# Performance work log

Measured on AMD Instinct MI355X. Metric: run time of the kernel, lower is better.

Reference implementation:

```python
import jax, jax.numpy as jnp
import numpy as np
from jax import lax

B, SEQ, PRED, CIN = 32, 336, 336, 7
ALL = SEQ + PRED
DM, DFF, NFFT, WIN, HOP = 64, 64, 64, 64, 8
NF = ALL // HOP + 1  # 85 STFT frames (center=True)
EL, CL, MARK = 2, 3, 4


def _conv2d(x, w, b, dil, pad):
    y = lax.conv_general_dilated(x, w, (1, 1), [(pad, pad), (pad, pad)],
                                 rhs_dilation=(dil, dil),
                                 dimension_numbers=('NCHW', 'OIHW', 'NCHW'))
    return y + b[None, :, None, None]


def _cconv(xr, xi, wr, wi, br, bi, dil, pad):
    # complex conv: (conv_r + i*conv_i)(xr + i*xi)
    rr = _conv2d(xr, wr, br, dil, pad)
    ii = _conv2d(xi, wi, bi, dil, pad)
    ri = _conv2d(xi, wr, br, dil, pad)
    ir = _conv2d(xr, wi, bi, dil, pad)
    return rr - ii, ri + ir


def _block(x, p):
    # x: [B, ALL, DM]; STFT per channel series (vectorized over B*DM, no python batch loop)
    xp = jnp.pad(x.transpose(0, 2, 1), ((0, 0), (0, 0), (NFFT // 2, NFFT // 2)), mode='reflect')
    idx = jnp.arange(NF)[:, None] * HOP + jnp.arange(NFFT)[None, :]
    win = 0.5 - 0.5 * jnp.cos(2.0 * jnp.pi * jnp.arange(WIN, dtype=jnp.float32) / WIN)  # periodic hann
    frames = xp[:, :, idx] * win  # [B, DM, NF, NFFT]
    S = jnp.fft.fft(frames, axis=-1) / jnp.sqrt(jnp.float32(NFFT))  # normalized=True (ortho)
    Sr = S.real.transpose(0, 1, 3, 2).astype(jnp.float32)  # [B, DM, NFFT, NF]
    Si = S.imag.transpose(0, 1, 3, 2).astype(jnp.float32)
    # complex 'qk' attention: compl_mul1d('ijxk,ijyk->ijxy', S, S)
    qk_r = jnp.einsum('bnxk,bnyk->bnxy', Sr, Sr) - jnp.einsum('bnxk,bnyk->bnxy', Si, Si)
    qk_i = jnp.einsum('bnxk,bnyk->bnxy', Sr, Si) + jnp.einsum('bnxk,bnyk->bnxy', Si, Sr)
    g_r = jax.nn.sigmoid(qk_r)
    g_i = jax.nn.sigmoid(qk_i)
    ar = jnp.einsum('bnxy,bnyz->bnxz', g_r, Sr) - jnp.einsum('bnxy,bnyz->bnxz', g_i, Si)
    ai = jnp.einsum('bnxy,bnyz->bnxz', g_r, Si) + jnp.einsum('bnxy,bnyz->bnxz', g_i, Sr)
    outs_r, outs_i = [], []
    yr, yi = _cconv(ar, ai, p['c0_wr'], p['c0_wi'], p['c0_br'], p['c0_bi'], 1, 0)
    outs_r.append(jax.nn.relu(yr)); outs_i.append(jax.nn.relu(yi))
    for k in range(1, CL):
        hr, hi = _cconv(ar, ai, p['cA_wr'][k - 1], p['cA_wi'][k - 1], p['cA_br'][k - 1], p['cA_bi'][k - 1], k, k)
        yr, yi = _cconv(hr, hi, p['cB_wr'][k - 1], p['cB_wi'][k - 1], p['cB_br'][k - 1], p['cB_bi'][k - 1], k, k)
        outs_r.append(jax.nn.relu(yr)); outs_i.append(jax.nn.relu(yi))
    mr = jnp.mean(jnp.stack(outs_r, -1), -1)
    mi = jnp.mean(jnp.stack(outs_i, -1), -1)
    y = mr * p['l0_w'][0, 0] + mi * p['l0_w'][0, 1] + p['l0_b'][0]  # Linear(2 -> 1) over (real, imag)
    y = y.mean(axis=2)  # mean over freq axis -> [B, DM, NF]
    y = jnp.einsum('bnf,af->bna', y, p['l2_w']) + p['l2_b']  # l2: NF -> ALL
    return y.transpose(0, 2, 1)  # [B, ALL, DM]


def _ln(x, g, b):
    m = x.mean(-1, keepdims=True)
    v = ((x - m) ** 2).mean(-1, keepdims=True)
    return (x - m) / jnp.sqrt(v + 1e-5) * g + b


def _forward(x_enc, x_mark_enc, tok_w, temp_w, pl_w, pl_b, ln_g, ln_b,
             c0_wr, c0_wi, c0_br, c0_bi, cA_wr, cA_wi, cA_br, cA_bi,
             cB_wr, cB_wi, cB_br, cB_bi, l0_w, l0_b, l2_w, l2_b,
             cv_w, cv_b, l1_w, l1_b, proj_w, proj_b):
    means = x_enc.mean(1, keepdims=True)
    xe = x_enc - means
    stdev = jnp.sqrt(xe.var(axis=1, keepdims=True) + 1e-5)
    xe = xe / stdev
    # DataEmbedding: circular token conv + sinusoidal PE + timeF linear (dropout=0)
    xv = jnp.pad(xe.transpose(0, 2, 1), ((0, 0), (0, 0), (1, 1)), mode='wrap')
    val = lax.conv_general_dilated(xv, tok_w, (1,), [(0, 0)],
                                   dimension_numbers=('NCH', 'OIH', 'NCH')).transpose(0, 2, 1)
    pos = jnp.arange(SEQ, dtype=jnp.float32)[:, None]
    div = jnp.exp(jnp.arange(0, DM, 2, dtype=jnp.float32) * (-np.log(10000.0) / DM))
    pe = jnp.zeros((SEQ, DM), jnp.float32).at[:, 0::2].set(jnp.sin(pos * div)).at[:, 1::2].set(jnp.cos(pos * div))
    enc = val + x_mark_enc @ temp_w.T + pe
    enc = jnp.einsum('btd,at->bad', enc, pl_w) + pl_b[None, :, None]  # predict_linear over time axis
    for l in range(EL):
        p = dict(c0_wr=c0_wr[l], c0_wi=c0_wi[l], c0_br=c0_br[l], c0_bi=c0_bi[l],
                 cA_wr=cA_wr[l], cA_wi=cA_wi[l], cA_br=cA_br[l], cA_bi=cA_bi[l],
                 cB_wr=cB_wr[l], cB_wi=cB_wi[l], cB_br=cB_br[l], cB_bi=cB_bi[l],
                 l0_w=l0_w[l], l0_b=l0_b[l], l2_w=l2_w[l], l2_b=l2_b[l])
        enc = _ln(_block(enc, p), ln_g, ln_b)
    # conv1d(in=ALL channels, kernel 3, stride 2, pad 1) over the d_model axis, then l1
    h = lax.conv_general_dilated(enc, cv_w, (2,), [(1, 1)],
                                 dimension_numbers=('NCH', 'OIH', 'NCH')) + cv_b[None, :, None]
    seq_series = (h @ l1_w.T)[..., 0] + l1_b[0]  # [B, ALL]
    dec = enc @ proj_w.T + proj_b
    dec = dec * stdev + means
    return dec[:, -PRED:, :], seq_series


def setup_inputs():
    key = jax.random.key(0)
    ks = jax.random.split(key, 24)
    def r(i, shape, s=0.02):
        return jax.random.normal(ks[i], shape, dtype=jnp.float32) * s
    return {
        'x_enc': jax.random.normal(ks[0], (B, SEQ, CIN), dtype=jnp.float32),
        'x_mark_enc': jax.random.normal(ks[1], (B, SEQ, MARK), dtype=jnp.float32),
        'x_dec': jax.random.normal(ks[2], (B, 48 + PRED, CIN), dtype=jnp.float32),
        'x_mark_dec': jax.random.normal(ks[3], (B, 48 + PRED, MARK), dtype=jnp.float32),
        'tok_w': r(4, (DM, CIN, 3), 0.1),
        'temp_w': r(5, (DM, MARK), 0.1),
        'pl_w': r(6, (ALL, SEQ), 0.05),
        'pl_b': jnp.zeros((ALL,), jnp.float32),
        'ln_g': jnp.ones((DM,), jnp.float32),
        'ln_b': jnp.zeros((DM,), jnp.float32),
        'c0_wr': r(7, (EL, DM, DM, 1, 1), 0.05),
        'c0_wi': r(8, (EL, DM, DM, 1, 1), 0.05),
        'c0_br': jnp.zeros((EL, DM), jnp.float32),
        'c0_bi': jnp.zeros((EL, DM), jnp.float32),
        'cA_wr': r(9, (EL, CL - 1, DFF, DM, 3, 3), 0.02),
        'cA_wi': r(10, (EL, CL - 1, DFF, DM, 3, 3), 0.02),
        'cA_br': jnp.zeros((EL, CL - 1, DFF), jnp.float32),
        'cA_bi': jnp.zeros((EL, CL - 1, DFF), jnp.float32),
        'cB_wr': r(11, (EL, CL - 1, DM, DFF, 3, 3), 0.02),
        'cB_wi': r(12, (EL, CL - 1, DM, DFF, 3, 3), 0.02),
        'cB_br': jnp.zeros((EL, CL - 1, DM), jnp.float32),
        'cB_bi': jnp.zeros((EL, CL - 1, DM), jnp.float32),
        'l0_w': r(13, (EL, 1, 2), 0.5),
        'l0_b': jnp.zeros((EL, 1), jnp.float32),
        'l2_w': r(14, (EL, ALL, NF), 0.05),
        'l2_b': jnp.zeros((EL, ALL), jnp.float32),
        'cv_w': r(15, (ALL, ALL, 3), 0.02),
        'cv_b': jnp.zeros((ALL,), jnp.float32),
        'l1_w': r(16, (1, DM // 2), 0.1),
        'l1_b': jnp.zeros((1,), jnp.float32),
        'proj_w': r(17, (CIN, DM), 0.1),
        'proj_b': jnp.zeros((CIN,), jnp.float32),
    }


def reference(x_enc, x_mark_enc, x_dec, x_mark_dec, tok_w, temp_w, pl_w, pl_b, ln_g, ln_b,
              c0_wr, c0_wi, c0_br, c0_bi, cA_wr, cA_wi, cA_br, cA_bi,
              cB_wr, cB_wi, cB_br, cB_bi, l0_w, l0_b, l2_w, l2_b,
              cv_w, cv_b, l1_w, l1_b, proj_w, proj_b):
    del x_dec, x_mark_dec  # unused in the forecast path
    return _forward(x_enc, x_mark_enc, tok_w, temp_w, pl_w, pl_b, ln_g, ln_b,
                    c0_wr, c0_wi, c0_br, c0_bi, cA_wr, cA_wi, cA_br, cA_bi,
                    cB_wr, cB_wi, cB_br, cB_bi, l0_w, l0_b, l2_w, l2_b,
                    cv_w, cv_b, l1_w, l1_b, proj_w, proj_b)
```

## Files before the change

kernel.cpp:

```cpp
#include <hip/hip_runtime.h>

typedef __attribute__((ext_vector_type(8))) short short8v;
typedef __attribute__((ext_vector_type(4))) float f32x4;
typedef __attribute__((ext_vector_type(16))) float f32x16;

static constexpr int Bt = 32;
static constexpr int SEQ = 336, PRED = 336, CIN = 7, ALLT = 672;
static constexpr int DM = 64, NFFT = 64, HOP = 8, NF = 85;
static constexpr int FPAD = 100;
static constexpr int MARK = 4;
static constexpr float INV3 = 1.0f / 3.0f;

__device__ inline short f2bf(float v) {
    unsigned u = __float_as_uint(v);
    u += 0x7fffu + ((u >> 16) & 1u);
    return (short)(u >> 16);
}
__device__ inline float bf2f(short h) {
    return __uint_as_float(((unsigned)(unsigned short)h) << 16);
}
__device__ inline int pack2(float r, float i) {
    return ((int)(unsigned short)f2bf(r)) | (((int)(unsigned short)f2bf(i)) << 16);
}
__device__ inline void async16(const int* g, short* l) {
    __builtin_amdgcn_global_load_lds(
        (const __attribute__((address_space(1))) unsigned int*)g,
        (__attribute__((address_space(3))) unsigned int*)l, 16, 0, 0);
}

__global__ __launch_bounds__(64) void k_stats(const float* __restrict__ x,
                                              float* __restrict__ mean,
                                              float* __restrict__ stdv) {
    int bc = blockIdx.x;
    int b = bc / CIN, c = bc % CIN;
    int lane = threadIdx.x;
    float s = 0.f, s2 = 0.f;
    for (int t = lane; t < SEQ; t += 64) {
        float v = x[(b * SEQ + t) * CIN + c];
        s += v; s2 += v * v;
    }
    for (int m = 32; m >= 1; m >>= 1) { s += __shfl_xor(s, m); s2 += __shfl_xor(s2, m); }
    if (lane == 0) {
        float mu = s / SEQ;
        float var = s2 / SEQ - mu * mu;
        mean[bc] = mu;
        stdv[bc] = sqrtf(var + 1e-5f);
    }
}

__global__ __launch_bounds__(256) void k_embed(const float* __restrict__ x,
                                               const float* __restrict__ mark,
                                               const float* __restrict__ tok_w,
                                               const float* __restrict__ temp_w,
                                               const float* __restrict__ mean,
                                               const float* __restrict__ stdv,
                                               float* __restrict__ enc0) {
    int i = blockIdx.x * 256 + threadIdx.x;
    if (i >= Bt * SEQ * DM) return;
    int d = i & 63;
    int t = (i >> 6) % SEQ;
    int b = i / (SEQ * DM);
    float val = 0.f;
    for (int c = 0; c < CIN; ++c) {
        float mu = mean[b * CIN + c];
        float is = 1.f / stdv[b * CIN + c];
        for (int j = 0; j < 3; ++j) {
            int tt = t + j - 1;
            if (tt < 0) tt += SEQ;
            if (tt >= SEQ) tt -= SEQ;
            float xv = (x[(b * SEQ + tt) * CIN + c] - mu) * is;
            val += xv * tok_w[(d * CIN + c) * 3 + j];
        }
    }
    float mk = 0.f;
    for (int m = 0; m < MARK; ++m) mk += mark[(b * SEQ + t) * MARK + m] * temp_w[d * MARK + m];
    float div = expf(-(float)(d & ~1) * (9.210340371976184f / (float)DM));
    float arg = (float)t * div;
    float pe = (d & 1) ? cosf(arg) : sinf(arg);
    enc0[i] = val + mk + pe;
}

__global__ __launch_bounds__(256) void k_plin2(const float* __restrict__ enc0,
                                               const float* __restrict__ pl_w,
                                               const float* __restrict__ pl_b,
                                               float* __restrict__ enc) {
    __shared__ float Et[56 * 64];
    __shared__ float Wt[56 * 49];
    int blk = blockIdx.x;
    int b = blk / 14, at = blk % 14;
    int abase = at * 48;
    int tid = threadIdx.x;
    int a0 = (tid & 15) * 3;
    int d0 = (tid >> 4) * 4;
    float acc[3][4];
#pragma unroll
    for (int q = 0; q < 3; ++q)
#pragma unroll
        for (int r = 0; r < 4; ++r) acc[q][r] = 0.f;
    for (int tc = 0; tc < 6; ++tc) {
        if (tc) __syncthreads();
        for (int i = tid; i < 56 * 64; i += 256)
            Et[i] = enc0[((size_t)b * SEQ + tc * 56) * DM + i];
        for (int i = tid; i < 48 * 56; i += 256) {
            int r = i / 56, c = i - r * 56;
            Wt[c * 49 + r] = pl_w[(size_t)(abase + r) * SEQ + tc * 56 + c];
        }
        __syncthreads();
#pragma unroll 4
        for (int t = 0; t < 56; ++t) {
            float4 e = *(const float4*)&Et[t * 64 + d0];
            float w0 = Wt[t * 49 + a0];
            float w1 = Wt[t * 49 + a0 + 1];
            float w2 = Wt[t * 49 + a0 + 2];
            acc[0][0] += w0 * e.x; acc[0][1] += w0 * e.y;
            acc[0][2] += w0 * e.z; acc[0][3] += w0 * e.w;
            acc[1][0] += w1 * e.x; acc[1][1] += w1 * e.y;
            acc[1][2] += w1 * e.z; acc[1][3] += w1 * e.w;
            acc[2][0] += w2 * e.x; acc[2][1] += w2 * e.y;
            acc[2][2] += w2 * e.z; acc[2][3] += w2 * e.w;
        }
    }
#pragma unroll
    for (int q = 0; q < 3; ++q) {
        int a = abase + a0 + q;
        float bias = pl_b[a];
        float4 o = {acc[q][0] + bias, acc[q][1] + bias, acc[q][2] + bias, acc[q][3] + bias};
        *(float4*)&enc[((size_t)b * ALLT + a) * DM + d0] = o;
    }
}

__global__ __launch_bounds__(512) void k_stqka(const float* __restrict__ enc, int b0,
                                               int* __restrict__ Apk) {
    __shared__ __align__(16) short L[54272];
    constexpr int TCH = 0, TCL = 4608, TSH = 9216, TSL = 13824;
    constexpr int XWH = 18432, XWL = 25344;
    float* xp  = (float*)&L[32256];
    float* twc = (float*)&L[33728];
    float* tws = (float*)&L[33984];
    constexpr int SRH = 0, SIH = 6656, SRL = 13312, SIL = 19968;
    constexpr int STRH = 26624, STRL = 33536, STIH = 40448, STIL = 47360;
    constexpr int GRH = 0, GRL = 4608, GIH = 9216, GIL = 13824;

    int blk = blockIdx.x;
    int bn = (blk & 7) * (gridDim.x >> 3) + (blk >> 3);
    int bl = bn >> 6, n = bn & 63;
    int bg = b0 + bl;
    int tid = threadIdx.x;
    int lane = tid & 63, w = tid >> 6;
    int l31 = lane & 31, kg = lane >> 5;

    for (int i = tid; i < ALLT + NFFT; i += 512) {
        int j = i - 32;
        if (j < 0) j = -j;
        if (j > ALLT - 1) j = 2 * (ALLT - 1) - j;
        xp[i] = enc[((size_t)bg * ALLT + j) * DM + n];
    }
    if (tid < 64) {
        float ang = (6.283185307179586f / 64.f) * (float)tid;
        twc[tid] = cosf(ang);
        tws[tid] = sinf(ang);
    }
    __syncthreads();
    for (int i = tid; i < 64 * 64; i += 512) {
        int k = i >> 6, tt = i & 63;
        int m = (k * tt) & 63;
        float c = twc[m], s = tws[m];
        short ch = f2bf(c); short cl = f2bf(c - bf2f(ch));
        short sh = f2bf(s); short sl = f2bf(s - bf2f(sh));
        int o = k * 72 + tt;
        L[TCH + o] = ch; L[TCL + o] = cl; L[TSH + o] = sh; L[TSL + o] = sl;
    }
    for (int i = tid; i < 96 * 64; i += 512) {
        int f = i >> 6, tt = i & 63;
        float v = 0.f;
        if (f < 85) v = xp[f * HOP + tt] * (0.5f - 0.5f * twc[tt]) * 0.125f;
        short vh = f2bf(v); short vl = f2bf(v - bf2f(vh));
        int o = f * 72 + tt;
        L[XWH + o] = vh; L[XWL + o] = vl;
    }
    __syncthreads();

    int kt = w & 1, ft = w >> 1;
    f32x16 sr, si;
#pragma unroll
    for (int r = 0; r < 16; ++r) { sr[r] = 0.f; si[r] = 0.f; }
    if (w < 6) {
#pragma unroll
        for (int tts = 0; tts < 4; ++tts) {
            int ko = (kt * 32 + l31) * 72 + tts * 16 + kg * 8;
            short8v ach = *(const short8v*)&L[TCH + ko];
            short8v acl = *(const short8v*)&L[TCL + ko];
            short8v ash = *(const short8v*)&L[TSH + ko];
            short8v asl = *(const short8v*)&L[TSL + ko];
            int bo = (ft * 32 + l31) * 72 + tts * 16 + kg * 8;
            short8v bh = *(const short8v*)&L[XWH + bo];
            short8v bl_ = *(const short8v*)&L[XWL + bo];
            sr = __builtin_amdgcn_mfma_f32_32x32x16_bf16(ach, bh, sr, 0, 0, 0);
            sr = __builtin_amdgcn_mfma_f32_32x32x16_bf16(acl, bh, sr, 0, 0, 0);
            sr = __builtin_amdgcn_mfma_f32_32x32x16_bf16(ach, bl_, sr, 0, 0, 0);
            si = __builtin_amdgcn_mfma_f32_32x32x16_bf16(ash, bh, si, 0, 0, 0);
            si = __builtin_amdgcn_mfma_f32_32x32x16_bf16(asl, bh, si, 0, 0, 0);
            si = __builtin_amdgcn_mfma_f32_32x32x16_bf16(ash, bl_, si, 0, 0, 0);
        }
    }
    __syncthreads();

    if (w < 6) {
        int fA = ft * 32 + l31;
#pragma unroll
        for (int rg = 0; rg < 4; ++rg) {
            int k0 = kt * 32 + 8 * rg + 4 * kg;
            short prh[4], prl[4], pih[4], pil[4];
#pragma unroll
            for (int q = 0; q < 4; ++q) {
                int r = rg * 4 + q;
                float sv = sr[r], iv = -si[r];
                short rh = f2bf(sv); short rl = f2bf(sv - bf2f(rh));
                short ih = f2bf(iv); short il = f2bf(iv - bf2f(ih));
                prh[q] = rh; prl[q] = rl; pih[q] = ih; pil[q] = il;
                L[SRH + (k0 + q) * 104 + fA] = rh; L[SRL + (k0 + q) * 104 + fA] = rl;
                L[SIH + (k0 + q) * 104 + fA] = ih; L[SIL + (k0 + q) * 104 + fA] = il;
            }
            *(long long*)&L[STRH + fA * 72 + k0] = *(long long*)prh;
            *(long long*)&L[STRL + fA * 72 + k0] = *(long long*)prl;
            *(long long*)&L[STIH + fA * 72 + k0] = *(long long*)pih;
            *(long long*)&L[STIL + fA * 72 + k0] = *(long long*)pil;
        }
    }
    __syncthreads();

    int mh = w >> 1, nh = w & 1;
    f32x16 P, Q, R;
#pragma unroll
    for (int r = 0; r < 16; ++r) { P[r] = 0.f; Q[r] = 0.f; R[r] = 0.f; }
    if (w < 4) {
#pragma unroll
        for (int f0 = 0; f0 < 96; f0 += 16) {
            int ka = f0 + kg * 8;
            int ra = (mh * 32 + l31) * 104 + ka;
            int rb = (nh * 32 + l31) * 104 + ka;
            short8v a_rh = *(const short8v*)&L[SRH + ra];
            short8v a_rl = *(const short8v*)&L[SRL + ra];
            short8v a_ih = *(const short8v*)&L[SIH + ra];
            short8v a_il = *(const short8v*)&L[SIL + ra];
            short8v b_rh = *(const short8v*)&L[SRH + rb];
            short8v b_rl = *(const short8v*)&L[SRL + rb];
            short8v b_ih = *(const short8v*)&L[SIH + rb];
            short8v b_il = *(const short8v*)&L[SIL + rb];
            P = __builtin_amdgcn_mfma_f32_32x32x16_bf16(a_rh, b_rh, P, 0, 0, 0);
            P = __builtin_amdgcn_mfma_f32_32x32x16_bf16(a_rl, b_rh, P, 0, 0, 0);
            P = __builtin_amdgcn_mfma_f32_32x32x16_bf16(a_rh, b_rl, P, 0, 0, 0);
            Q = __builtin_amdgcn_mfma_f32_32x32x16_bf16(a_ih, b_ih, Q, 0, 0, 0);
            Q = __builtin_amdgcn_mfma_f32_32x32x16_bf16(a_il, b_ih, Q, 0, 0, 0);
            Q = __builtin_amdgcn_mfma_f32_32x32x16_bf16(a_ih, b_il, Q, 0, 0, 0);
            R = __builtin_amdgcn_mfma_f32_32x32x16_bf16(a_rh, b_ih, R, 0, 0, 0);
            R = __builtin_amdgcn_mfma_f32_32x32x16_bf16(a_rl, b_ih, R, 0, 0, 0);
            R = __builtin_amdgcn_mfma_f32_32x32x16_bf16(a_rh, b_il, R, 0, 0, 0);
            R = __builtin_amdgcn_mfma_f32_32x32x16_bf16(a_ih, b_rh, R, 0, 0, 0);
            R = __builtin_amdgcn_mfma_f32_32x32x16_bf16(a_il, b_rh, R, 0, 0, 0);
            R = __builtin_amdgcn_mfma_f32_32x32x16_bf16(a_ih, b_rl, R, 0, 0, 0);
        }
    }
    __syncthreads();

    if (w < 4) {
        int y = nh * 32 + l31;
#pragma unroll
        for (int r = 0; r < 16; ++r) {
            int x = mh * 32 + (r & 3) + 8 * (r >> 2) + 4 * kg;
            float gr = 1.f / (1.f + __expf(-(P[r] - Q[r])));
            float gi = 1.f / (1.f + __expf(-R[r]));
            short gh = f2bf(gr); short gl = f2bf(gr - bf2f(gh));
            short jh = f2bf(gi); short jl = f2bf(gi - bf2f(jh));
            L[GRH + x * 72 + y] = gh; L[GRL + x * 72 + y] = gl;
            L[GIH + x * 72 + y] = jh; L[GIL + x * 72 + y] = jl;
        }
    }
    __syncthreads();

    int mt = w >> 1, nx = w & 1;
    f32x16 u1, u2, u3;
#pragma unroll
    for (int r = 0; r < 16; ++r) { u1[r] = 0.f; u2[r] = 0.f; u3[r] = 0.f; }
    if (w < 6) {
#pragma unroll
        for (int y0 = 0; y0 < 64; y0 += 16) {
            int kb = y0 + kg * 8;
            int gb = (nx * 32 + l31) * 72 + kb;
            short8v bgrh = *(const short8v*)&L[GRH + gb];
            short8v bgrl = *(const short8v*)&L[GRL + gb];
            short8v bgih = *(const short8v*)&L[GIH + gb];
            short8v bgil = *(const short8v*)&L[GIL + gb];
            int sa = (mt * 32 + l31) * 72 + kb;
            short8v arh = *(const short8v*)&L[STRH + sa];
            short8v arl = *(const short8v*)&L[STRL + sa];
            short8v aih = *(const short8v*)&L[STIH + sa];
            short8v ail = *(const short8v*)&L[STIL + sa];
            u1 = __builtin_amdgcn_mfma_f32_32x32x16_bf16(arh, bgrh, u1, 0, 0, 0);
            u1 = __builtin_amdgcn_mfma_f32_32x32x16_bf16(arl, bgrh, u1, 0, 0, 0);
            u1 = __builtin_amdgcn_mfma_f32_32x32x16_bf16(arh, bgrl, u1, 0, 0, 0);
            u2 = __builtin_amdgcn_mfma_f32_32x32x16_bf16(aih, bgih, u2, 0, 0, 0);
            u2 = __builtin_amdgcn_mfma_f32_32x32x16_bf16(ail, bgih, u2, 0, 0, 0);
            u2 = __builtin_amdgcn_mfma_f32_32x32x16_bf16(aih, bgil, u2, 0, 0, 0);
            u3 = __builtin_amdgcn_mfma_f32_32x32x16_bf16(aih, bgrh, u3, 0, 0, 0);
            u3 = __builtin_amdgcn_mfma_f32_32x32x16_bf16(ail, bgrh, u3, 0, 0, 0);
            u3 = __builtin_amdgcn_mfma_f32_32x32x16_bf16(aih, bgrl, u3, 0, 0, 0);
            u3 = __builtin_amdgcn_mfma_f32_32x32x16_bf16(arh, bgih, u3, 0, 0, 0);
            u3 = __builtin_amdgcn_mfma_f32_32x32x16_bf16(arl, bgih, u3, 0, 0, 0);
            u3 = __builtin_amdgcn_mfma_f32_32x32x16_bf16(arh, bgil, u3, 0, 0, 0);
        }
    }
    if (w < 6) {
        size_t pkbase = ((size_t)(bl * 16 + (n >> 2)) * 64) * FPAD * 4 + (n & 3);
        int x2 = nx * 32 + l31;
#pragma unroll
        for (int r = 0; r < 16; ++r) {
            int z = mt * 32 + (r & 3) + 8 * (r >> 2) + 4 * kg;
            if (z < 85)
                Apk[pkbase + ((size_t)x2 * FPAD + z + 2) * 4] = pack2(u1[r] - u2[r], u3[r]);
        }
    }
}

__global__ __launch_bounds__(256) void k_wprep(const float* __restrict__ cA_wr,
                                               const float* __restrict__ cA_wi,
                                               const float* __restrict__ cB_wr,
                                               const float* __restrict__ cB_wi,
                                               const float* __restrict__ c0_wr,
                                               const float* __restrict__ c0_wi,
                                               short* __restrict__ wt) {
    int idx = blockIdx.x * 256 + threadIdx.x;
    if (idx >= 1245184) return;
    int c32 = idx & 31;
    int m = (idx >> 5) & 127;
    int ci_l = c32 >> 1;
    int part = c32 & 1;
    int co = m & 63;
    const float *wr, *wi;
    size_t woff;
    bool lo = false;
    int chunk;
    if (idx < 1179648) {
        chunk = (idx >> 12) & 3;
        int tap = (idx >> 14) % 9;
        int conv = idx / 147456;
        int l = conv >> 2, k1 = (conv >> 1) & 1, ab = conv & 1;
        int ci = chunk * 16 + ci_l;
        woff = (((size_t)(l * 2 + k1) * 64 + co) * 64 + ci) * 9 + tap;
        wr = ab ? cB_wr : cA_wr;
        wi = ab ? cB_wi : cA_wi;
    } else {
        int i2 = idx - 1179648;
        chunk = (i2 >> 12) & 3;
        lo = (i2 >> 14) & 1;
        int l = i2 >> 15;
        int ci = chunk * 16 + ci_l;
        woff = ((size_t)(l * 64 + co)) * 64 + ci;
        wr = c0_wr; wi = c0_wi;
    }
    float a = wr[woff], bb = wi[woff];
    float v = (m < 64) ? (part ? -bb : a) : (part ? a : bb);
    if (lo) v = v - bf2f(f2bf(v));
    wt[idx] = f2bf(v);
}

__global__ __launch_bounds__(256, 4) void k_conv3p(const int* __restrict__ in_pk,
                                                   const short* __restrict__ wt,
                                                   const float* __restrict__ b_r,
                                                   const float* __restrict__ b_i,
                                                   int K, int mode,
                                                   const float* __restrict__ l0w,
                                                   int* __restrict__ out_pk,
                                                   float* __restrict__ yfull) {
    __shared__ __align__(16) short inT[2][1200 * 8];
    int blk = blockIdx.x;
    int swz = (blk & 7) * (gridDim.x >> 3) + (blk >> 3);
    int b = swz >> 6, x0 = swz & 63;
    int tid = threadIdx.x;
    int lane = tid & 63, wid = tid >> 6;
    int wrow = wid & 1, wcol = wid >> 1;
    int l15 = lane & 15, g = lane >> 4;

#define STAGE(CC, BUFI)                                                       \
    do {                                                                      \
        _Pragma("unroll")                                                     \
        for (int it = 0; it < 5; ++it) {                                      \
            int idx = tid + it * 256;                                         \
            if (idx < 1200) {                                                 \
                int f = idx % FPAD;                                           \
                int rc = idx / FPAD;                                          \
                int xr = rc >> 2, cg = rc & 3;                                \
                int xg = x0 + (xr - 1) * K;                                   \
                if ((unsigned)xg < 64u) {                                     \
                    const int* src = in_pk +                                  \
                        (((size_t)((b * 16 + (CC) * 4 + cg) * 64 + xg)) * FPAD + f) * 4; \
                    async16(src, &inT[BUFI][(wid * 64 + it * 256) * 8]);      \
                }                                                             \
            }                                                                 \
        }                                                                     \
    } while (0)

    { int* p = (int*)&inT[0][0];
      for (int i = tid; i < 2 * 1200 * 4; i += 256) p[i] = 0; }
    __syncthreads();

    f32x4 acc[4][3];
#pragma unroll
    for (int a = 0; a < 4; ++a)
#pragma unroll
        for (int j = 0; j < 3; ++j) acc[a][j] = f32x4{0.f, 0.f, 0.f, 0.f};

    STAGE(0, 0);
    __syncthreads();

    int cur = 0;
    for (int chunk = 0; chunk < 4; ++chunk) {
        if (chunk == 0) STAGE(1, 1);
        else if (chunk == 1) STAGE(2, 0);
        else if (chunk == 2) STAGE(3, 1);
        const short* bb = &inT[cur][0];
#pragma unroll
        for (int u = 0; u < 3; ++u) {
#pragma unroll
            for (int v = 0; v < 3; ++v) {
                int tap = u * 3 + v;
                short8v afr[4];
#pragma unroll
                for (int a = 0; a < 4; ++a) {
                    int tile = (a < 2) ? (wrow * 2 + a) : (wrow * 2 + a + 2);
                    const short* ap = wt + ((((size_t)tap * 4 + chunk) * 8 + tile) * 16 + l15) * 32 + g * 8;
                    afr[a] = *(const short8v*)ap;
                }
                short8v bfr[3];
#pragma unroll
                for (int j = 0; j < 3; ++j) {
                    int fs2 = (wcol * 3 + j) * 16 + l15 + (v - 1) * K + 2;
                    bfr[j] = *(const short8v*)&bb[((u * 4 + g) * FPAD + fs2) * 8];
                }
#pragma unroll
                for (int a = 0; a < 4; ++a)
#pragma unroll
                    for (int j = 0; j < 3; ++j)
                        acc[a][j] = __builtin_amdgcn_mfma_f32_16x16x32_bf16(afr[a], bfr[j],
                                                                            acc[a][j], 0, 0, 0);
            }
        }
        __syncthreads();
        cur ^= 1;
    }
#undef STAGE

    float w0 = 0.f, w1 = 0.f;
    if (mode == 1) { w0 = l0w[0]; w1 = l0w[1]; }
#pragma unroll
    for (int a = 0; a < 2; ++a) {
#pragma unroll
        for (int j = 0; j < 3; ++j) {
            int f = (wcol * 3 + j) * 16 + l15;
            if (f < NF) {
                if (mode == 0) {
                    int4 o;
#pragma unroll
                    for (int reg = 0; reg < 4; ++reg) {
                        int co = (wrow * 2 + a) * 16 + g * 4 + reg;
                        float vrq = acc[a][j][reg]     + b_r[co] - b_i[co];
                        float viq = acc[a + 2][j][reg] + b_r[co] + b_i[co];
                        ((int*)&o)[reg] = pack2(vrq, viq);
                    }
                    int co4 = (wrow * 2 + a) * 4 + g;
                    ((int4*)out_pk)[((size_t)((b * 16 + co4) * 64 + x0)) * FPAD + f + 2] = o;
                } else {
#pragma unroll
                    for (int reg = 0; reg < 4; ++reg) {
                        int co = (wrow * 2 + a) * 16 + g * 4 + reg;
                        float vrq = acc[a][j][reg]     + b_r[co] - b_i[co];
                        float viq = acc[a + 2][j][reg] + b_r[co] + b_i[co];
                        size_t o = ((size_t)(b * 64 + co) * 64 + x0) * NF + f;
                        yfull[o] += (fmaxf(vrq, 0.f) * w0 + fmaxf(viq, 0.f) * w1) * INV3;
                    }
                }
            }
        }
    }
}

__global__ __launch_bounds__(256, 4) void k_c0m(const int* __restrict__ Apk,
                                                const short* __restrict__ wt,
                                                const float* __restrict__ b_r,
                                                const float* __restrict__ b_i,
                                                const float* __restrict__ l0w,
                                                float* __restrict__ yfull) {
    __shared__ __align__(16) short inT[100 * 40];
    int blk = blockIdx.x;
    int swz = (blk & 7) * (gridDim.x >> 3) + (blk >> 3);
    int b = swz >> 6, x0 = swz & 63;
    int tid = threadIdx.x;
    int lane = tid & 63, wid = tid >> 6;
    int wrow = wid & 1, wcol = wid >> 1;
    int l15 = lane & 15, g = lane >> 4;

    f32x4 acc[4][3];
#pragma unroll
    for (int a = 0; a < 4; ++a)
#pragma unroll
        for (int j = 0; j < 3; ++j) acc[a][j] = f32x4{0.f, 0.f, 0.f, 0.f};

    for (int chunk = 0; chunk < 4; ++chunk) {
        if (chunk > 0) __syncthreads();
        for (int idx = tid; idx < 400; idx += 256) {
            int f = idx % FPAD;
            int cg = idx / FPAD;
            size_t s4 = ((size_t)((b * 16 + chunk * 4 + cg) * 64 + x0)) * FPAD + f;
            int4 dh = ((const int4*)Apk)[s4];
            *(int4*)&inT[f * 40 + cg * 8] = dh;
        }
        __syncthreads();
#pragma unroll
        for (int wtap = 0; wtap < 2; ++wtap) {
            short8v afr[4];
#pragma unroll
            for (int a = 0; a < 4; ++a) {
                int tile = (a < 2) ? (wrow * 2 + a) : (wrow * 2 + a + 2);
                const short* ap = wt + ((((size_t)wtap * 4 + chunk) * 8 + tile) * 16 + l15) * 32 + g * 8;
                afr[a] = *(const short8v*)ap;
            }
            short8v bfr[3];
#pragma unroll
            for (int j = 0; j < 3; ++j) {
                int fs = (wcol * 3 + j) * 16 + l15 + 2;
                bfr[j] = *(const short8v*)&inT[fs * 40 + g * 8];
            }
#pragma unroll
            for (int a = 0; a < 4; ++a)
#pragma unroll
                for (int j = 0; j < 3; ++j)
                    acc[a][j] = __builtin_amdgcn_mfma_f32_16x16x32_bf16(afr[a], bfr[j],
                                                                        acc[a][j], 0, 0, 0);
        }
    }

    float w0 = l0w[0], w1 = l0w[1];
#pragma unroll
    for (int a = 0; a < 2; ++a) {
#pragma unroll
        for (int j = 0; j < 3; ++j) {
            int f = (wcol * 3 + j) * 16 + l15;
            if (f < NF) {
#pragma unroll
                for (int reg = 0; reg < 4; ++reg) {
                    int co = (wrow * 2 + a) * 16 + g * 4 + reg;
                    float vrq = acc[a][j][reg]     + b_r[co] - b_i[co];
                    float viq = acc[a + 2][j][reg] + b_r[co] + b_i[co];
                    size_t o = ((size_t)(b * 64 + co) * 64 + x0) * NF + f;
                    yfull[o] = (fmaxf(vrq, 0.f) * w0 + fmaxf(viq, 0.f) * w1) * INV3;
                }
            }
        }
    }
}

__global__ __launch_bounds__(256) void k_reduce2(const float* __restrict__ yfull,
                                                 const float* __restrict__ l0b,
                                                 float* __restrict__ y2) {
    __shared__ float fs[3][85];
    int bn = blockIdx.x;
    int tid = threadIdx.x;
    const float* p = yfull + (size_t)bn * 64 * 85;
    if (tid < 255) {
        int f = tid % 85, g = tid / 85;
        float s = 0.f;
        for (int x = g; x < 64; x += 3) s += p[x * 85 + f];
        fs[g][f] = s;
    }
    __syncthreads();
    if (tid < 85)
        y2[(size_t)bn * 85 + tid] = (fs[0][tid] + fs[1][tid] + fs[2][tid]) * (1.f / 64.f) + l0b[0];
}

__global__ __launch_bounds__(64) void k_l2ln(const float* __restrict__ y2,
                                             const float* __restrict__ l2w,
                                             const float* __restrict__ l2b,
                                             const float* __restrict__ g,
                                             const float* __restrict__ be,
                                             float* __restrict__ enc, int b0) {
    int bl = blockIdx.x / ALLT;
    int a = blockIdx.x % ALLT;
    int d = threadIdx.x;
    const float* wp = l2w + (size_t)a * NF;
    const float* yp = y2 + (size_t)(bl * 64 + d) * NF;
    float acc = l2b[a];
    for (int f = 0; f < NF; ++f) acc += yp[f] * wp[f];
    float s = acc, s2 = acc * acc;
    for (int m = 32; m >= 1; m >>= 1) { s += __shfl_xor(s, m); s2 += __shfl_xor(s2, m); }
    float mu = s * (1.f / 64.f);
    float var = s2 * (1.f / 64.f) - mu * mu;
    float rs = rsqrtf(var + 1e-5f);
    enc[((size_t)(b0 + bl) * ALLT + a) * DM + d] = (acc - mu) * rs * g[d] + be[d];
}

__global__ __launch_bounds__(256) void k_T(const float* __restrict__ enc,
                                           const float* __restrict__ l1w,
                                           float* __restrict__ T) {
    int i = blockIdx.x * 256 + threadIdx.x;
    if (i >= Bt * ALLT * 3) return;
    int j = i % 3;
    int rest = i / 3;
    int ci = rest % ALLT;
    int b = rest / ALLT;
    const float* e = enc + ((size_t)b * ALLT + ci) * DM;
    float s = 0.f;
    for (int hx = 0; hx < 32; ++hx) {
        int p = 2 * hx + j - 1;
        if (p >= 0 && p < DM) s += e[p] * l1w[hx];
    }
    T[i] = s;
}

__global__ __launch_bounds__(256) void k_seq(const float* __restrict__ T,
                                             const float* __restrict__ cvw,
                                             const float* __restrict__ cvb,
                                             const float* __restrict__ l1w,
                                             const float* __restrict__ l1b,
                                             float* __restrict__ out) {
    int i = blockIdx.x * 256 + threadIdx.x;
    if (i >= Bt * ALLT) return;
    int co = i % ALLT;
    int b = i / ALLT;
    float sl1 = 0.f;
    for (int hx = 0; hx < 32; ++hx) sl1 += l1w[hx];
    const float* tp = T + (size_t)b * ALLT * 3;
    const float* wp = cvw + (size_t)co * ALLT * 3;
    float s = 0.f;
    for (int q = 0; q < ALLT * 3; ++q) s += tp[q] * wp[q];
    out[i] = s + cvb[co] * sl1 + l1b[0];
}

__global__ __launch_bounds__(256) void k_dec(const float* __restrict__ enc,
                                             const float* __restrict__ pw,
                                             const float* __restrict__ pb,
                                             const float* __restrict__ mean,
                                             const float* __restrict__ stdv,
                                             float* __restrict__ out) {
    int i = blockIdx.x * 256 + threadIdx.x;
    if (i >= Bt * PRED * CIN) return;
    int c = i % CIN;
    int rest = i / CIN;
    int tt = rest % PRED;
    int b = rest / PRED;
    const float* e = enc + ((size_t)b * ALLT + SEQ + tt) * DM;
    const float* w = pw + c * DM;
    float s = pb[c];
    for (int d = 0; d < DM; ++d) s += e[d] * w[d];
    out[i] = s * stdv[b * CIN + c] + mean[b * CIN + c];
}

extern "C" void kernel_launch(void* const* d_in, const int* in_sizes, int n_in,
                              void* d_out, int out_size, void* d_ws, size_t ws_size,
                              hipStream_t stream) {
    (void)in_sizes; (void)n_in; (void)out_size;
    const float* x_enc  = (const float*)d_in[0];
    const float* x_mark = (const float*)d_in[1];
    const float* tok_w  = (const float*)d_in[4];
    const float* temp_w = (const float*)d_in[5];
    const float* pl_w   = (const float*)d_in[6];
    const float* pl_b   = (const float*)d_in[7];
    const float* ln_g   = (const float*)d_in[8];
    const float* ln_b   = (const float*)d_in[9];
    const float* c0_wr  = (const float*)d_in[10];
    const float* c0_wi  = (const float*)d_in[11];
    const float* c0_br  = (const float*)d_in[12];
    const float* c0_bi  = (const float*)d_in[13];
    const float* cA_wr  = (const float*)d_in[14];
    const float* cA_wi  = (const float*)d_in[15];
    const float* cA_br  = (const float*)d_in[16];
    const float* cA_bi  = (const float*)d_in[17];
    const float* cB_wr  = (const float*)d_in[18];
    const float* cB_wi  = (const float*)d_in[19];
    const float* cB_br  = (const float*)d_in[20];
    const float* cB_bi  = (const float*)d_in[21];
    const float* l0_w   = (const float*)d_in[22];
    const float* l0_b   = (const float*)d_in[23];
    const float* l2_w   = (const float*)d_in[24];
    const float* l2_b   = (const float*)d_in[25];
    const float* cv_w   = (const float*)d_in[26];
    const float* cv_b   = (const float*)d_in[27];
    const float* l1_w   = (const float*)d_in[28];
    const float* l1_b   = (const float*)d_in[29];
    const float* proj_w = (const float*)d_in[30];
    const float* proj_b = (const float*)d_in[31];

    float* out0 = (float*)d_out;
    float* out1 = out0 + (size_t)Bt * PRED * CIN;

    float* ws = (float*)d_ws;
    size_t off = 0;
    float* enc  = ws + off; off += (size_t)Bt * ALLT * DM;
    float* enc0 = ws + off; off += (size_t)Bt * SEQ * DM;
    float* mean = ws + off; off += 256;
    float* stdv = ws + off; off += 256;
    short* wtbuf = (short*)(ws + off); off += 622592;

    const size_t perb = (size_t)DM * NFFT * NF;
    const size_t perbp = (size_t)16 * 64 * FPAD * 4;
    int Bc = 32;
    while (Bc > 1) {
        size_t need = (off + (size_t)Bc * (DM * NF + perb + 2 * perbp)) * sizeof(float);
        if (need <= ws_size) break;
        Bc >>= 1;
    }
    float* y2 = ws + off; off += (size_t)Bc * DM * NF;
    float* yfull = ws + off; off += (size_t)Bc * perb;
    int*   Apk = (int*)(ws + off); off += (size_t)Bc * perbp;
    int*   Hpk = (int*)(ws + off); off += (size_t)Bc * perbp;
    float* Tb = enc0;

    hipMemsetAsync(Apk, 0, (size_t)Bc * perbp * 2 * sizeof(int), stream);

    k_stats<<<Bt * CIN, 64, 0, stream>>>(x_enc, mean, stdv);
    k_wprep<<<(1245184 + 255) / 256, 256, 0, stream>>>(cA_wr, cA_wi, cB_wr, cB_wi,
                                                       c0_wr, c0_wi, wtbuf);
    k_embed<<<(Bt * SEQ * DM + 255) / 256, 256, 0, stream>>>(x_enc, x_mark, tok_w, temp_w,
                                                             mean, stdv, enc0);
    k_plin2<<<Bt * 14, 256, 0, stream>>>(enc0, pl_w, pl_b, enc);

    for (int l = 0; l < 2; ++l) {
        for (int b0 = 0; b0 < Bt; b0 += Bc) {
            k_stqka<<<Bc * 64, 512, 0, stream>>>(enc, b0, Apk);
            k_c0m<<<Bc * 64, 256, 0, stream>>>(Apk, wtbuf + 1179648 + (size_t)l * 32768,
                                               c0_br + l * 64, c0_bi + l * 64,
                                               l0_w + l * 2, yfull);
            for (int k = 1; k <= 2; ++k) {
                int convA = l * 4 + (k - 1) * 2;
                size_t boff = ((size_t)l * 2 + (k - 1)) * 64;
                k_conv3p<<<Bc * 64, 256, 0, stream>>>(Apk, wtbuf + (size_t)convA * 147456,
                                                      cA_br + boff, cA_bi + boff, k, 0,
                                                      l0_w + l * 2, Hpk, yfull);
                k_conv3p<<<Bc * 64, 256, 0, stream>>>(Hpk, wtbuf + (size_t)(convA + 1) * 147456,
                                                      cB_br + boff, cB_bi + boff, k, 1,
                                                      l0_w + l * 2, Hpk, yfull);
            }
            k_reduce2<<<Bc * 64, 256, 0, stream>>>(yfull, l0_b + l, y2);
            k_l2ln<<<Bc * ALLT, 64, 0, stream>>>(y2, l2_w + (size_t)l * ALLT * NF,
                                                 l2_b + (size_t)l * ALLT, ln_g, ln_b, enc, b0);
        }
    }

    k_T<<<(Bt * ALLT * 3 + 255) / 256, 256, 0, stream>>>(enc, l1_w, Tb);
    k_seq<<<(Bt * ALLT + 255) / 256, 256, 0, stream>>>(Tb, cv_w, cv_b, l1_w, l1_b, out1);
    k_dec<<<(Bt * PRED * CIN + 255) / 256, 256, 0, stream>>>(enc, proj_w, proj_b, mean, stdv, out0);
}
```

Measured before the change: 1.382 ms.

## Precompute DFT twiddles globally, transpose enc for coalesced loads, zero only pads

Moves the per-block twiddle and Hann-window generation into a one-time k_twprep kernel whose bf16 hi/lo tables each block copies with 16-byte loads. Adds a k_encT transpose so each block's per-channel series loads contiguously instead of with a 64-float stride. Replaces the full memset of the Apk/Hpk buffers with a kernel that zeroes only the padding columns. The cost is an extra transpose launch per layer and chunk, plus the assumption that the padding columns are the only part of those buffers that must start at zero.

```diff
diff --git a/kernel.cpp b/kernel.cpp
--- a/kernel.cpp
+++ b/kernel.cpp
@@ -129,14 +129,60 @@
     }
 }
 
-__global__ __launch_bounds__(512) void k_stqka(const float* __restrict__ enc, int b0,
-                                               int* __restrict__ Apk) {
+__global__ __launch_bounds__(256) void k_twprep(short* __restrict__ twg) {
+    int idx = blockIdx.x * 256 + threadIdx.x;
+    if (idx < 18432) {
+        int arr = idx / 4608;
+        int rem = idx - arr * 4608;
+        int k = rem / 72, tt = rem - k * 72;
+        float v = 0.f;
+        if (tt < 64) {
+            int m = (k * tt) & 63;
+            float ang = (6.283185307179586f / 64.f) * (float)m;
+            float c = (arr < 2) ? cosf(ang) : sinf(ang);
+            v = (arr & 1) ? (c - bf2f(f2bf(c))) : c;
+        }
+        twg[idx] = f2bf(v);
+    } else if (idx < 18432 + 64) {
+        int tt = idx - 18432;
+        float ang = (6.283185307179586f / 64.f) * (float)tt;
+        ((float*)(twg + 18432))[tt] = (0.5f - 0.5f * cosf(ang)) * 0.125f;
+    }
+}
+
+__global__ __launch_bounds__(256) void k_encT(const float* __restrict__ enc,
+                                              float* __restrict__ encT) {
+    __shared__ float tile[64][65];
+    int b = blockIdx.x / 11, tt0 = (blockIdx.x % 11) * 64;
+    int tid = threadIdx.x;
+    int tx = tid & 63, ty = tid >> 6;
+    for (int r = ty; r < 64; r += 4) {
+        int t = tt0 + r;
+        if (t < ALLT) tile[r][tx] = enc[((size_t)b * ALLT + t) * DM + tx];
+    }
+    __syncthreads();
+    for (int r = ty; r < 64; r += 4) {
+        int t = tt0 + tx;
+        if (t < ALLT) encT[((size_t)b * DM + r) * ALLT + t] = tile[tx][r];
+    }
+}
+
+__global__ __launch_bounds__(256) void k_padzero(int4* __restrict__ base, int nrows) {
+    int idx = blockIdx.x * 256 + threadIdx.x;
+    if (idx >= nrows * 15) return;
+    int r = idx / 15, p = idx - r * 15;
+    int f = (p < 2) ? p : (85 + p);
+    base[(size_t)r * FPAD + f] = int4{0, 0, 0, 0};
+}
+
+__global__ __launch_bounds__(512) void k_stqka(const float* __restrict__ encT, int b0,
+                                               int* __restrict__ Apk,
+                                               const short* __restrict__ twg) {
     __shared__ __align__(16) short L[54272];
     constexpr int TCH = 0, TCL = 4608, TSH = 9216, TSL = 13824;
     constexpr int XWH = 18432, XWL = 25344;
     float* xp  = (float*)&L[32256];
-    float* twc = (float*)&L[33728];
-    float* tws = (float*)&L[33984];
+    float* win = (float*)&L[33728];
     constexpr int SRH = 0, SIH = 6656, SRL = 13312, SIL = 19968;
     constexpr int STRH = 26624, STRL = 33536, STIH = 40448, STIL = 47360;
     constexpr int GRH = 0, GRL = 4608, GIH = 9216, GIL = 13824;
@@ -153,27 +199,16 @@
         int j = i - 32;
         if (j < 0) j = -j;
         if (j > ALLT - 1) j = 2 * (ALLT - 1) - j;
-        xp[i] = enc[((size_t)bg * ALLT + j) * DM + n];
-    }
-    if (tid < 64) {
-        float ang = (6.283185307179586f / 64.f) * (float)tid;
-        twc[tid] = cosf(ang);
-        tws[tid] = sinf(ang);
-    }
-    __syncthreads();
-    for (int i = tid; i < 64 * 64; i += 512) {
-        int k = i >> 6, tt = i & 63;
-        int m = (k * tt) & 63;
-        float c = twc[m], s = tws[m];
-        short ch = f2bf(c); short cl = f2bf(c - bf2f(ch));
-        short sh = f2bf(s); short sl = f2bf(s - bf2f(sh));
-        int o = k * 72 + tt;
-        L[TCH + o] = ch; L[TCL + o] = cl; L[TSH + o] = sh; L[TSL + o] = sl;
-    }
+        xp[i] = encT[(size_t)(bg * 64 + n) * ALLT + j];
+    }
+    for (int i = tid; i < 2304; i += 512)
+        *(int4*)&L[i * 8] = ((const int4*)twg)[i];
+    if (tid < 64) win[tid] = ((const float*)(twg + 18432))[tid];
+    __syncthreads();
     for (int i = tid; i < 96 * 64; i += 512) {
         int f = i >> 6, tt = i & 63;
         float v = 0.f;
-        if (f < 85) v = xp[f * HOP + tt] * (0.5f - 0.5f * twc[tt]) * 0.125f;
+        if (f < 85) v = xp[f * HOP + tt] * win[tt];
         short vh = f2bf(v); short vl = f2bf(v - bf2f(vh));
         int o = f * 72 + tt;
         L[XWH + o] = vh; L[XWL + o] = vl;
@@ -695,10 +730,12 @@
     float* ws = (float*)d_ws;
     size_t off = 0;
     float* enc  = ws + off; off += (size_t)Bt * ALLT * DM;
+    float* encT = ws + off; off += (size_t)Bt * ALLT * DM;
     float* enc0 = ws + off; off += (size_t)Bt * SEQ * DM;
     float* mean = ws + off; off += 256;
     float* stdv = ws + off; off += 256;
     short* wtbuf = (short*)(ws + off); off += 622592;
+    short* twg   = (short*)(ws + off); off += 9600;
 
     const size_t perb = (size_t)DM * NFFT * NF;
     const size_t perbp = (size_t)16 * 64 * FPAD * 4;
@@ -714,18 +751,22 @@
     int*   Hpk = (int*)(ws + off); off += (size_t)Bc * perbp;
     float* Tb = enc0;
 
-    hipMemsetAsync(Apk, 0, (size_t)Bc * perbp * 2 * sizeof(int), stream);
-
     k_stats<<<Bt * CIN, 64, 0, stream>>>(x_enc, mean, stdv);
+    k_twprep<<<(18432 + 64 + 255) / 256, 256, 0, stream>>>(twg);
     k_wprep<<<(1245184 + 255) / 256, 256, 0, stream>>>(cA_wr, cA_wi, cB_wr, cB_wi,
                                                        c0_wr, c0_wi, wtbuf);
+    {
+        int nrows = 2 * Bc * 16 * 64;
+        k_padzero<<<(nrows * 15 + 255) / 256, 256, 0, stream>>>((int4*)Apk, nrows);
+    }
     k_embed<<<(Bt * SEQ * DM + 255) / 256, 256, 0, stream>>>(x_enc, x_mark, tok_w, temp_w,
                                                              mean, stdv, enc0);
     k_plin2<<<Bt * 14, 256, 0, stream>>>(enc0, pl_w, pl_b, enc);
 
     for (int l = 0; l < 2; ++l) {
         for (int b0 = 0; b0 < Bt; b0 += Bc) {
-            k_stqka<<<Bc * 64, 512, 0, stream>>>(enc, b0, Apk);
+            k_encT<<<Bt * 11, 256, 0, stream>>>(enc, encT);
+            k_stqka<<<Bc * 64, 512, 0, stream>>>(encT, b0, Apk, twg);
             k_c0m<<<Bc * 64, 256, 0, stream>>>(Apk, wtbuf + 1179648 + (size_t)l * 32768,
                                                c0_br + l * 64, c0_bi + l * 64,
                                                l0_w + l * 2, yfull);
```

Result: no change. 1.379 ms (-0.2%).
